# Kernel optimization log

Hardware: AMD Instinct MI355X
Metric: run time of the kernel (lower is better)

The kernel has to match this reference:

```python
import jax, jax.numpy as jnp
import numpy as np

EMB = 768

def _mlp2(x, Wa, Wb):
    # relu(LL2(relu(LL1(x)))), bias-free linears stored as [out, in]
    return jax.nn.relu(jax.nn.relu(x @ Wa.T) @ Wb.T)

def setup_inputs() -> dict:
    key = jax.random.key(0)
    ks = jax.random.split(key, 6)
    n, m = 16, 4096  # maxlen = 64 paragraphs -> 64*64 pair slots
    X_data = jax.random.normal(ks[0], (n, 1 + m, 3 * EMB), dtype=jnp.float32)
    # first token carries num_clusters metadata (unused by the differentiable path)
    W1 = jax.random.normal(ks[1], (256, EMB), dtype=jnp.float32) * 0.02
    W2 = jax.random.normal(ks[2], (128, 256), dtype=jnp.float32) * 0.02
    W3 = jax.random.normal(ks[3], (256, EMB), dtype=jnp.float32) * 0.02
    W4 = jax.random.normal(ks[4], (128, 256), dtype=jnp.float32) * 0.02
    W5 = jax.random.normal(ks[5], (1, 128), dtype=jnp.float32) * 0.02
    return {"X_data": X_data, "W1": W1, "W2": W2, "W3": W3, "W4": W4, "W5": W5}

def reference(X_data, W1, W2, W3, W4, W5):
    # CATSCluster differentiable path: QueryScaler on X_data[:, 1:, :]
    X = X_data[:, 1:, :]                      # [n, m, 3*EMB]
    Xq = X[..., :EMB]
    Xp1 = X[..., EMB:2 * EMB]
    Xp2 = X[..., 2 * EMB:]
    Xp1z = _mlp2(Xp1, W1, W2)                 # [n, m, 128]
    Xp2z = _mlp2(Xp2, W1, W2)
    Xqz = _mlp2(Xq, W3, W4)
    Xpqz = Xqz * jnp.abs(Xp1z - Xp2z)         # [n, m, 128]
    dist = jnp.tanh(jax.nn.relu(Xpqz @ W5.T))[..., 0]  # [n, m]
    n, m = dist.shape
    p = int(np.sqrt(m))                       # maxlen
    # batch_pairscore_matrix fed to the host-side clustering step
    return dist.reshape(n, p, p)
```

## Files before the change

### kernel.cpp

```cpp
#include <hip/hip_runtime.h>


typedef short short8 __attribute__((ext_vector_type(8)));
typedef float f32x4 __attribute__((ext_vector_type(4)));

#define W1H_OFF 0u
#define W1L_OFF 196608u
#define W3H_OFF 393216u
#define W3L_OFF 589824u
#define W2H_OFF 786432u
#define W2L_OFF 819200u
#define W4H_OFF 851968u
#define W4L_OFF 884736u

__device__ __forceinline__ unsigned short bf16_rne(float f) {
  unsigned int u = __float_as_uint(f);
  u += 0x7FFFu + ((u >> 16) & 1u);
  return (unsigned short)(u >> 16);
}

__device__ __forceinline__ void split_bf16(float f, unsigned short& h, unsigned short& l) {
  h = bf16_rne(f);
  float fh = __uint_as_float(((unsigned int)h) << 16);
  l = bf16_rne(f - fh);
}

__global__ __launch_bounds__(256) void prep_weights(
    const float* __restrict__ W1, const float* __restrict__ W2,
    const float* __restrict__ W3, const float* __restrict__ W4,
    unsigned short* __restrict__ ws)
{
  int i = blockIdx.x * 256 + threadIdx.x;
  if (i < 196608) {
    unsigned short h, l;
    split_bf16(W1[i], h, l); ws[W1H_OFF + i] = h; ws[W1L_OFF + i] = l;
    split_bf16(W3[i], h, l); ws[W3H_OFF + i] = h; ws[W3L_OFF + i] = l;
    if (i < 32768) {
      split_bf16(W2[i], h, l); ws[W2H_OFF + i] = h; ws[W2L_OFF + i] = l;
      split_bf16(W4[i], h, l); ws[W4H_OFF + i] = h; ws[W4L_OFF + i] = l;
    }
  }
}

#define STRIDE_A 40
#define STRIDE_H 264

__global__ __launch_bounds__(512, 4) void catsc_main(
    const float* __restrict__ X, const unsigned short* __restrict__ ws,
    const float* __restrict__ W5, float* __restrict__ out)
{
  __shared__ short lsA[2][2][64 * STRIDE_A];
  __shared__ short lsH[64 * STRIDE_H];
  __shared__ float lsPart[8][64];

  const int tid  = threadIdx.x;
  const int wave = tid >> 6;
  const int lane = tid & 63;
  const int l15  = lane & 15;
  const int q    = lane >> 4;
  const int blk  = blockIdx.x;

  const float* Xb = X + (size_t)((blk >> 6) * 4097 + 1 + ((blk & 63) << 6)) * 2304;

  const int srow = tid >> 3;
  const int f4   = (tid & 7) << 2;

  f32x4 zp[4];

#pragma unroll
  for (int s = 0; s < 3; ++s) {
    const int so = (s == 0) ? 768 : (s == 1) ? 1536 : 0;
    const unsigned short* B1h = ws + (s == 2 ? W3H_OFF : W1H_OFF);
    const unsigned short* B1l = ws + (s == 2 ? W3L_OFF : W1L_OFF);
    const unsigned short* B2h = ws + (s == 2 ? W4H_OFF : W2H_OFF);
    const unsigned short* B2l = ws + (s == 2 ? W4L_OFF : W2L_OFF);

    const float* Xrow = Xb + (size_t)srow * 2304 + so + f4;

    f32x4 acc[4][2];
#pragma unroll
    for (int m = 0; m < 4; ++m)
#pragma unroll
      for (int n = 0; n < 2; ++n)
        acc[m][n] = f32x4{0.f, 0.f, 0.f, 0.f};

    {
      float4 v0 = *(const float4*)(Xrow);
      unsigned short h0,h1,h2,h3,l0,l1,l2,l3;
      split_bf16(v0.x,h0,l0); split_bf16(v0.y,h1,l1);
      split_bf16(v0.z,h2,l2); split_bf16(v0.w,h3,l3);
      uint2 ph, pl;
      ph.x = (unsigned)h0 | ((unsigned)h1 << 16); ph.y = (unsigned)h2 | ((unsigned)h3 << 16);
      pl.x = (unsigned)l0 | ((unsigned)l1 << 16); pl.y = (unsigned)l2 | ((unsigned)l3 << 16);
      *(uint2*)&lsA[0][0][srow * STRIDE_A + f4] = ph;
      *(uint2*)&lsA[0][1][srow * STRIDE_A + f4] = pl;
    }
    float4 vB = *(const float4*)(Xrow + 32);
    __syncthreads();

    for (int c = 0; c < 24; ++c) {
      const int b = c & 1;

      const int cl = (c + 2 < 24) ? (c + 2) : 23;
      float4 vN = *(const float4*)(Xrow + cl * 32);

      short8 Bh[2], Bl[2];
#pragma unroll
      for (int n = 0; n < 2; ++n) {
        size_t off = (size_t)((wave * 2 + n) * 16 + l15) * 768 + c * 32 + q * 8;
        Bh[n] = *(const short8*)(B1h + off);
        Bl[n] = *(const short8*)(B1l + off);
      }
      short8 Ah[4], Al[4];
#pragma unroll
      for (int m = 0; m < 4; ++m) {
        int a = (m * 16 + l15) * STRIDE_A + q * 8;
        Ah[m] = *(const short8*)&lsA[b][0][a];
        Al[m] = *(const short8*)&lsA[b][1][a];
      }

      if (c + 1 < 24) {
        unsigned short h0,h1,h2,h3,l0,l1,l2,l3;
        split_bf16(vB.x,h0,l0); split_bf16(vB.y,h1,l1);
        split_bf16(vB.z,h2,l2); split_bf16(vB.w,h3,l3);
        uint2 ph, pl;
        ph.x = (unsigned)h0 | ((unsigned)h1 << 16); ph.y = (unsigned)h2 | ((unsigned)h3 << 16);
        pl.x = (unsigned)l0 | ((unsigned)l1 << 16); pl.y = (unsigned)l2 | ((unsigned)l3 << 16);
        const int wb = b ^ 1;
        *(uint2*)&lsA[wb][0][srow * STRIDE_A + f4] = ph;
        *(uint2*)&lsA[wb][1][srow * STRIDE_A + f4] = pl;
      }

#pragma unroll
      for (int m = 0; m < 4; ++m)
#pragma unroll
        for (int n = 0; n < 2; ++n)
          acc[m][n] = __builtin_amdgcn_mfma_f32_16x16x32_bf16(Ah[m], Bh[n], acc[m][n], 0, 0, 0);
#pragma unroll
      for (int m = 0; m < 4; ++m)
#pragma unroll
        for (int n = 0; n < 2; ++n)
          acc[m][n] = __builtin_amdgcn_mfma_f32_16x16x32_bf16(Ah[m], Bl[n], acc[m][n], 0, 0, 0);
#pragma unroll
      for (int m = 0; m < 4; ++m)
#pragma unroll
        for (int n = 0; n < 2; ++n)
          acc[m][n] = __builtin_amdgcn_mfma_f32_16x16x32_bf16(Al[m], Bh[n], acc[m][n], 0, 0, 0);

      __syncthreads();
      vB = vN;
    }

#pragma unroll
    for (int m = 0; m < 4; ++m)
#pragma unroll
      for (int n = 0; n < 2; ++n) {
        int col = (wave * 2 + n) * 16 + l15;
#pragma unroll
        for (int i = 0; i < 4; ++i) {
          int row = m * 16 + q * 4 + i;
          lsH[row * STRIDE_H + col] = bf16_rne(fmaxf(acc[m][n][i], 0.f));
        }
      }
    __syncthreads();

    f32x4 acc2[4];
#pragma unroll
    for (int m = 0; m < 4; ++m) acc2[m] = f32x4{0.f, 0.f, 0.f, 0.f};

    for (int c2 = 0; c2 < 8; ++c2) {
      size_t off = (size_t)(wave * 16 + l15) * 256 + c2 * 32 + q * 8;
      short8 Ch = *(const short8*)(B2h + off);
      short8 Cl = *(const short8*)(B2l + off);
      short8 Ha[4];
#pragma unroll
      for (int m = 0; m < 4; ++m)
        Ha[m] = *(const short8*)&lsH[(m * 16 + l15) * STRIDE_H + c2 * 32 + q * 8];
#pragma unroll
      for (int m = 0; m < 4; ++m)
        acc2[m] = __builtin_amdgcn_mfma_f32_16x16x32_bf16(Ha[m], Ch, acc2[m], 0, 0, 0);
#pragma unroll
      for (int m = 0; m < 4; ++m)
        acc2[m] = __builtin_amdgcn_mfma_f32_16x16x32_bf16(Ha[m], Cl, acc2[m], 0, 0, 0);
    }

    if (s == 0) {
#pragma unroll
      for (int m = 0; m < 4; ++m)
#pragma unroll
        for (int i = 0; i < 4; ++i)
          zp[m][i] = fmaxf(acc2[m][i], 0.f);
    } else if (s == 1) {
#pragma unroll
      for (int m = 0; m < 4; ++m)
#pragma unroll
        for (int i = 0; i < 4; ++i)
          zp[m][i] = fabsf(zp[m][i] - fmaxf(acc2[m][i], 0.f));
    } else {
      const float w5c = W5[wave * 16 + l15];
#pragma unroll
      for (int m = 0; m < 4; ++m)
#pragma unroll
        for (int i = 0; i < 4; ++i) {
          float v = fmaxf(acc2[m][i], 0.f) * zp[m][i] * w5c;
          v += __shfl_xor(v, 1);
          v += __shfl_xor(v, 2);
          v += __shfl_xor(v, 4);
          v += __shfl_xor(v, 8);
          if (l15 == 0) lsPart[wave][m * 16 + q * 4 + i] = v;
        }
    }
  }

  __syncthreads();
  if (tid < 64) {
    float sum = lsPart[0][tid] + lsPart[1][tid] + lsPart[2][tid] + lsPart[3][tid]
              + lsPart[4][tid] + lsPart[5][tid] + lsPart[6][tid] + lsPart[7][tid];
    out[(size_t)blk * 64 + tid] = tanhf(fmaxf(sum, 0.f));
  }
}

extern "C" void kernel_launch(void* const* d_in, const int* in_sizes, int n_in,
                              void* d_out, int out_size, void* d_ws, size_t ws_size,
                              hipStream_t stream) {
  const float* X  = (const float*)d_in[0];
  const float* W1 = (const float*)d_in[1];
  const float* W2 = (const float*)d_in[2];
  const float* W3 = (const float*)d_in[3];
  const float* W4 = (const float*)d_in[4];
  const float* W5 = (const float*)d_in[5];
  float* out = (float*)d_out;
  unsigned short* ws = (unsigned short*)d_ws;

  prep_weights<<<dim3(768), dim3(256), 0, stream>>>(W1, W2, W3, W4, ws);
  catsc_main<<<dim3(1024), dim3(512), 0, stream>>>(X, ws, W5, out);
}
```

Baseline: 1.090 ms.

## Double K-chunk to 64 per barrier and prefetch next stage's first tile

```diff
diff --git a/kernel.cpp b/kernel.cpp
--- a/kernel.cpp
+++ b/kernel.cpp
@@ -23,6 +23,14 @@
   h = bf16_rne(f);
   float fh = __uint_as_float(((unsigned int)h) << 16);
   l = bf16_rne(f - fh);
+}
+
+__device__ __forceinline__ void pack_split4(const float4 v, uint2& ph, uint2& pl) {
+  unsigned short h0,h1,h2,h3,l0,l1,l2,l3;
+  split_bf16(v.x,h0,l0); split_bf16(v.y,h1,l1);
+  split_bf16(v.z,h2,l2); split_bf16(v.w,h3,l3);
+  ph.x = (unsigned)h0 | ((unsigned)h1 << 16); ph.y = (unsigned)h2 | ((unsigned)h3 << 16);
+  pl.x = (unsigned)l0 | ((unsigned)l1 << 16); pl.y = (unsigned)l2 | ((unsigned)l3 << 16);
 }
 
 __global__ __launch_bounds__(256) void prep_weights(
@@ -42,7 +50,7 @@
   }
 }
 
-#define STRIDE_A 40
+#define STRIDE_A 72
 #define STRIDE_H 264
 
 __global__ __launch_bounds__(512, 4) void catsc_main(
@@ -63,9 +71,16 @@
   const float* Xb = X + (size_t)((blk >> 6) * 4097 + 1 + ((blk & 63) << 6)) * 2304;
 
   const int srow = tid >> 3;
-  const int f4   = (tid & 7) << 2;
+  const int scol = (tid & 7) << 3;
+  const float* Xs = Xb + (size_t)srow * 2304 + scol;
+  short* lsW = &lsA[0][0][0];
+  const int sidx = srow * STRIDE_A + scol;
+  const int PLANE = 64 * STRIDE_A;
 
   f32x4 zp[4];
+
+  float4 vP0 = *(const float4*)(Xs + 768);
+  float4 vP1 = *(const float4*)(Xs + 768 + 4);
 
 #pragma unroll
   for (int s = 0; s < 3; ++s) {
@@ -75,8 +90,6 @@
     const unsigned short* B2h = ws + (s == 2 ? W4H_OFF : W2H_OFF);
     const unsigned short* B2l = ws + (s == 2 ? W4L_OFF : W2L_OFF);
 
-    const float* Xrow = Xb + (size_t)srow * 2304 + so + f4;
-
     f32x4 acc[4][2];
 #pragma unroll
     for (int m = 0; m < 4; ++m)
@@ -85,70 +98,72 @@
         acc[m][n] = f32x4{0.f, 0.f, 0.f, 0.f};
 
     {
-      float4 v0 = *(const float4*)(Xrow);
-      unsigned short h0,h1,h2,h3,l0,l1,l2,l3;
-      split_bf16(v0.x,h0,l0); split_bf16(v0.y,h1,l1);
-      split_bf16(v0.z,h2,l2); split_bf16(v0.w,h3,l3);
       uint2 ph, pl;
-      ph.x = (unsigned)h0 | ((unsigned)h1 << 16); ph.y = (unsigned)h2 | ((unsigned)h3 << 16);
-      pl.x = (unsigned)l0 | ((unsigned)l1 << 16); pl.y = (unsigned)l2 | ((unsigned)l3 << 16);
-      *(uint2*)&lsA[0][0][srow * STRIDE_A + f4] = ph;
-      *(uint2*)&lsA[0][1][srow * STRIDE_A + f4] = pl;
-    }
-    float4 vB = *(const float4*)(Xrow + 32);
+      pack_split4(vP0, ph, pl);
+      *(uint2*)&lsW[sidx]         = ph;
+      *(uint2*)&lsW[PLANE + sidx] = pl;
+      pack_split4(vP1, ph, pl);
+      *(uint2*)&lsW[sidx + 4]         = ph;
+      *(uint2*)&lsW[PLANE + sidx + 4] = pl;
+    }
     __syncthreads();
 
-    for (int c = 0; c < 24; ++c) {
-      const int b = c & 1;
-
-      const int cl = (c + 2 < 24) ? (c + 2) : 23;
-      float4 vN = *(const float4*)(Xrow + cl * 32);
-
-      short8 Bh[2], Bl[2];
-#pragma unroll
-      for (int n = 0; n < 2; ++n) {
-        size_t off = (size_t)((wave * 2 + n) * 16 + l15) * 768 + c * 32 + q * 8;
-        Bh[n] = *(const short8*)(B1h + off);
-        Bl[n] = *(const short8*)(B1l + off);
-      }
-      short8 Ah[4], Al[4];
-#pragma unroll
-      for (int m = 0; m < 4; ++m) {
-        int a = (m * 16 + l15) * STRIDE_A + q * 8;
-        Ah[m] = *(const short8*)&lsA[b][0][a];
-        Al[m] = *(const short8*)&lsA[b][1][a];
-      }
-
-      if (c + 1 < 24) {
-        unsigned short h0,h1,h2,h3,l0,l1,l2,l3;
-        split_bf16(vB.x,h0,l0); split_bf16(vB.y,h1,l1);
-        split_bf16(vB.z,h2,l2); split_bf16(vB.w,h3,l3);
+    for (int p = 0; p < 12; ++p) {
+      const int b = p & 1;
+      float4 vB0, vB1;
+      if (p + 1 < 12) {
+        vB0 = *(const float4*)(Xs + so + (p + 1) * 64);
+        vB1 = *(const float4*)(Xs + so + (p + 1) * 64 + 4);
+      }
+
+#pragma unroll
+      for (int sub = 0; sub < 2; ++sub) {
+        short8 Bh[2], Bl[2];
+#pragma unroll
+        for (int n = 0; n < 2; ++n) {
+          size_t off = (size_t)((wave * 2 + n) * 16 + l15) * 768 + p * 64 + sub * 32 + q * 8;
+          Bh[n] = *(const short8*)(B1h + off);
+          Bl[n] = *(const short8*)(B1l + off);
+        }
+#pragma unroll
+        for (int mh = 0; mh < 2; ++mh) {
+          short8 Ah[2], Al[2];
+#pragma unroll
+          for (int mm = 0; mm < 2; ++mm) {
+            int a = ((mh * 2 + mm) * 16 + l15) * STRIDE_A + sub * 32 + q * 8;
+            Ah[mm] = *(const short8*)&lsA[b][0][a];
+            Al[mm] = *(const short8*)&lsA[b][1][a];
+          }
+#pragma unroll
+          for (int mm = 0; mm < 2; ++mm)
+#pragma unroll
+            for (int n = 0; n < 2; ++n)
+              acc[mh*2+mm][n] = __builtin_amdgcn_mfma_f32_16x16x32_bf16(Ah[mm], Bh[n], acc[mh*2+mm][n], 0, 0, 0);
+#pragma unroll
+          for (int mm = 0; mm < 2; ++mm)
+#pragma unroll
+            for (int n = 0; n < 2; ++n)
+              acc[mh*2+mm][n] = __builtin_amdgcn_mfma_f32_16x16x32_bf16(Ah[mm], Bl[n], acc[mh*2+mm][n], 0, 0, 0);
+#pragma unroll
+          for (int mm = 0; mm < 2; ++mm)
+#pragma unroll
+            for (int n = 0; n < 2; ++n)
+              acc[mh*2+mm][n] = __builtin_amdgcn_mfma_f32_16x16x32_bf16(Al[mm], Bh[n], acc[mh*2+mm][n], 0, 0, 0);
+        }
+      }
+
+      if (p + 1 < 12) {
+        const int wb = b ^ 1;
+        short* dst = &lsA[wb][0][0];
         uint2 ph, pl;
-        ph.x = (unsigned)h0 | ((unsigned)h1 << 16); ph.y = (unsigned)h2 | ((unsigned)h3 << 16);
-        pl.x = (unsigned)l0 | ((unsigned)l1 << 16); pl.y = (unsigned)l2 | ((unsigned)l3 << 16);
-        const int wb = b ^ 1;
-        *(uint2*)&lsA[wb][0][srow * STRIDE_A + f4] = ph;
-        *(uint2*)&lsA[wb][1][srow * STRIDE_A + f4] = pl;
-      }
-
-#pragma unroll
-      for (int m = 0; m < 4; ++m)
-#pragma unroll
-        for (int n = 0; n < 2; ++n)
-          acc[m][n] = __builtin_amdgcn_mfma_f32_16x16x32_bf16(Ah[m], Bh[n], acc[m][n], 0, 0, 0);
-#pragma unroll
-      for (int m = 0; m < 4; ++m)
-#pragma unroll
-        for (int n = 0; n < 2; ++n)
-          acc[m][n] = __builtin_amdgcn_mfma_f32_16x16x32_bf16(Ah[m], Bl[n], acc[m][n], 0, 0, 0);
-#pragma unroll
-      for (int m = 0; m < 4; ++m)
-#pragma unroll
-        for (int n = 0; n < 2; ++n)
-          acc[m][n] = __builtin_amdgcn_mfma_f32_16x16x32_bf16(Al[m], Bh[n], acc[m][n], 0, 0, 0);
-
+        pack_split4(vB0, ph, pl);
+        *(uint2*)&dst[sidx]         = ph;
+        *(uint2*)&dst[PLANE + sidx] = pl;
+        pack_split4(vB1, ph, pl);
+        *(uint2*)&dst[sidx + 4]         = ph;
+        *(uint2*)&dst[PLANE + sidx + 4] = pl;
+      }
       __syncthreads();
-      vB = vN;
     }
 
 #pragma unroll
@@ -163,6 +178,14 @@
         }
       }
     __syncthreads();
+
+    if (s == 0) {
+      vP0 = *(const float4*)(Xs + 1536);
+      vP1 = *(const float4*)(Xs + 1536 + 4);
+    } else if (s == 1) {
+      vP0 = *(const float4*)(Xs);
+      vP1 = *(const float4*)(Xs + 4);
+    }
 
     f32x4 acc2[4];
 #pragma unroll
```

Result: faster. 1.062 ms (-2.6%).
